# Kernel tuning notes

Measured on AMD Instinct MI355X. Metric: run time of the kernel, lower is better.

The kernel has to match this reference:

```python
import jax, jax.numpy as jnp
import numpy as np

WS = 8          # window size (== stride, non-overlapping)
C_IN = 256
RED = 8
C_QK = C_IN // RED  # 32


def setup_inputs() -> dict:
    key = jax.random.key(0)
    ks = jax.random.split(key, 8)
    B, C, H, W = 4, C_IN, 256, 256
    x = jax.random.normal(ks[0], (B, C, H, W), dtype=jnp.float32)
    # 1x1 conv weights stored as [out_ch, in_ch] (kaiming-ish scale)
    wq = jax.random.normal(ks[1], (C_QK, C), dtype=jnp.float32) * np.sqrt(2.0 / C)
    wk = jax.random.normal(ks[2], (C_QK, C), dtype=jnp.float32) * np.sqrt(2.0 / C)
    wv = jax.random.normal(ks[3], (C, C), dtype=jnp.float32) * np.sqrt(2.0 / C)
    bq = jnp.zeros((C_QK,), dtype=jnp.float32)
    bk = jnp.zeros((C_QK,), dtype=jnp.float32)
    bv = jnp.zeros((C,), dtype=jnp.float32)
    gamma = jax.random.normal(ks[4], (1,), dtype=jnp.float32) * 0.5
    return {"x": x, "wq": wq, "bq": bq, "wk": wk, "bk": bk,
            "wv": wv, "bv": bv, "gamma": gamma}


def reference(x, wq, bq, wk, bk, wv, bv, gamma):
    B, C, H, W = x.shape
    Hw, Ww = H // WS, W // WS
    P = WS * WS  # 64 pixels per window
    # extract non-overlapping windows: [B,C,H,W] -> [N, C, P]
    xw = x.reshape(B, C, Hw, WS, Ww, WS)
    xw = xw.transpose(0, 2, 4, 1, 3, 5).reshape(B * Hw * Ww, C, P)
    # 1x1 conv projections (per-pixel channel GEMM)
    q = jnp.einsum('ncp,oc->nop', xw, wq) + bq[None, :, None]   # [N, Cqk, P]
    k = jnp.einsum('ncp,oc->nop', xw, wk) + bk[None, :, None]   # [N, Cqk, P]
    v = jnp.einsum('ncp,oc->nop', xw, wv) + bv[None, :, None]   # [N, C,   P]
    # attn[p, q_] = <Q[:,p], K[:,q_]> / sqrt(P), softmax over q_
    scale = 1.0 / np.sqrt(float(P))
    attn = jax.nn.softmax(jnp.einsum('ncp,ncq->npq', q, k) * scale, axis=-1)
    # out = V @ attn^T : out[c,p] = sum_q V[c,q] * attn[p,q]
    out = jnp.einsum('ncq,npq->ncp', v, attn)  # [N, C, P]
    # merge windows back: [N, C, P] -> [B, C, H, W]
    out = out.reshape(B, Hw, Ww, C, WS, WS)
    out = out.transpose(0, 3, 1, 4, 2, 5).reshape(B, C, H, W)
    return gamma * out + x
```

## Files before the change

### kernel.cpp

```cpp
#include <hip/hip_runtime.h>
#include <hip/hip_bf16.h>
#include <stdint.h>


#define CIN    256
#define WIMG   256
#define CH_STRIDE 65536

typedef __bf16 bf16x8 __attribute__((ext_vector_type(8)));
typedef float  f32x4  __attribute__((ext_vector_type(4)));

#define XT_OFF 0
#define QT_OFF 16384
#define KT_OFF 20480
#define PT_OFF 16384
#define HALF_LDS 24576

__device__ __forceinline__ int swz8(int p) { return (p ^ (p >> 3)) & 7; }

__device__ __forceinline__ uint32_t pack2(float lo, float hi) {
  union { __bf16 h[2]; uint32_t u; } un;
  un.h[0] = (__bf16)lo; un.h[1] = (__bf16)hi;
  return un.u;
}

union fragu { uint32_t u[4]; bf16x8 v; };

__global__ __launch_bounds__(256) void wprep_kernel(
    const float* __restrict__ wq, const float* __restrict__ wk,
    const float* __restrict__ wv, __bf16* __restrict__ out)
{
  int i = blockIdx.x * 256 + threadIdx.x;
  int off = i * 4;
  const float* src;
  if (off < 8192)       src = wq + off;
  else if (off < 16384) src = wk + (off - 8192);
  else                  src = wv + (off - 16384);
  float4 v = *(const float4*)src;
  __bf16 h[4] = {(__bf16)v.x, (__bf16)v.y, (__bf16)v.z, (__bf16)v.w};
  *(uint2*)(out + off) = *(const uint2*)h;
}

__global__ __launch_bounds__(512) void win_attn_kernel(
    const float* __restrict__ x,  const __bf16* __restrict__ wsb,
    const float* __restrict__ bq, const float* __restrict__ bk,
    const float* __restrict__ bv, const float* __restrict__ gamma,
    float* __restrict__ out, int nblk)
{
  __shared__ __attribute__((aligned(16))) unsigned char lds_raw[2 * HALF_LDS];

  int t = threadIdx.x;
  int half = t >> 8;
  int tt = t & 255;
  unsigned char* ldsb = lds_raw + half * HALF_LDS;

  int bid   = blockIdx.x;
  int chunkb = nblk >> 3;
  int swz   = (bid & 7) * chunkb + (bid >> 3);
  int b   = swz >> 9;
  int hw  = (swz >> 4) & 31;
  int wwp = swz & 15;
  int ww  = wwp * 2 + half;
  size_t win_off = (size_t)b * (CIN * CH_STRIDE) + (size_t)hw * 8 * WIMG + (size_t)ww * 8;
  const float* xw = x + win_off;
  float* ow = out + win_off;

  int w = tt >> 6, l = tt & 63, l16 = l & 15, lq = l >> 4;
  float g = gamma[0];

  int qkrow = (w & 1) * 16;
  f32x4 qacc[4]    = {};
  f32x4 vacc[4][4] = {};
  const __bf16* wqkrow = wsb + ((w < 2) ? 0 : 8192) + (qkrow + l16) * 256 + lq * 8;
  const __bf16* vrow   = wsb + 16384 + (w * 64 + l16) * 256 + lq * 8;

  #pragma unroll
  for (int it = 0; it < 4; ++it) {
    int id   = it * 256 + tt;
    int hf   = id & 1;
    int i    = (id >> 1) & 7;
    int c2   = id >> 4;
    const float* r0 = xw + (size_t)(2 * c2) * CH_STRIDE + i * WIMG + hf * 4;
    float4 va = *(const float4*)r0;
    float4 vb = *(const float4*)(r0 + CH_STRIDE);
    float ax[4] = {va.x, va.y, va.z, va.w};
    float bx[4] = {vb.x, vb.y, vb.z, vb.w};
    int blk = c2 >> 2;
    int sub = (c2 & 3) * 4;
    #pragma unroll
    for (int jj = 0; jj < 4; ++jj) {
      int p = i * 8 + hf * 4 + jj;
      *(uint32_t*)(ldsb + XT_OFF + p * 256 + ((blk ^ swz8(p)) << 4) + sub) =
          pack2(ax[jj], bx[jj]);
    }
  }
  __syncthreads();

  float4 pfa[4], pfb[4];
  #pragma unroll
  for (int it = 0; it < 4; ++it) {
    int id   = it * 256 + tt;
    int hf   = id & 1;
    int i    = (id >> 1) & 7;
    int c2   = id >> 4;
    const float* r0 = xw + (size_t)(128 + 2 * c2) * CH_STRIDE + i * WIMG + hf * 4;
    pfa[it] = *(const float4*)r0;
    pfb[it] = *(const float4*)(r0 + CH_STRIDE);
  }

  #pragma unroll
  for (int ks = 0; ks < 4; ++ks) {
    bf16x8 wvf[4];
    #pragma unroll
    for (int ci = 0; ci < 4; ++ci)
      wvf[ci] = *(const bf16x8*)(vrow + ci * 16 * 256 + ks * 32);
    bf16x8 wqkf = *(const bf16x8*)(wqkrow + ks * 32);
    bf16x8 xb[4];
    #pragma unroll
    for (int qi = 0; qi < 4; ++qi) {
      int p = qi * 16 + l16;
      xb[qi] = *(const bf16x8*)(ldsb + XT_OFF + p * 256 +
                                (((ks * 4 + lq) ^ swz8(p)) << 4));
    }
    #pragma unroll
    for (int qi = 0; qi < 4; ++qi)
      qacc[qi] = __builtin_amdgcn_mfma_f32_16x16x32_bf16(wqkf, xb[qi], qacc[qi], 0, 0, 0);
    #pragma unroll
    for (int ci = 0; ci < 4; ++ci) {
      #pragma unroll
      for (int pi = 0; pi < 4; ++pi)
        vacc[pi][ci] = __builtin_amdgcn_mfma_f32_16x16x32_bf16(xb[pi], wvf[ci], vacc[pi][ci], 0, 0, 0);
    }
  }
  __syncthreads();

  #pragma unroll
  for (int it = 0; it < 4; ++it) {
    int id   = it * 256 + tt;
    int hf   = id & 1;
    int i    = (id >> 1) & 7;
    int c2   = id >> 4;
    float ax[4] = {pfa[it].x, pfa[it].y, pfa[it].z, pfa[it].w};
    float bx[4] = {pfb[it].x, pfb[it].y, pfb[it].z, pfb[it].w};
    int blk = c2 >> 2;
    int sub = (c2 & 3) * 4;
    #pragma unroll
    for (int jj = 0; jj < 4; ++jj) {
      int p = i * 8 + hf * 4 + jj;
      *(uint32_t*)(ldsb + XT_OFF + p * 256 + ((blk ^ swz8(p)) << 4) + sub) =
          pack2(ax[jj], bx[jj]);
    }
  }
  __syncthreads();

  #pragma unroll
  for (int ks = 0; ks < 4; ++ks) {
    bf16x8 wvf[4];
    #pragma unroll
    for (int ci = 0; ci < 4; ++ci)
      wvf[ci] = *(const bf16x8*)(vrow + ci * 16 * 256 + 128 + ks * 32);
    bf16x8 wqkf = *(const bf16x8*)(wqkrow + 128 + ks * 32);
    bf16x8 xb[4];
    #pragma unroll
    for (int qi = 0; qi < 4; ++qi) {
      int p = qi * 16 + l16;
      xb[qi] = *(const bf16x8*)(ldsb + XT_OFF + p * 256 +
                                (((ks * 4 + lq) ^ swz8(p)) << 4));
    }
    #pragma unroll
    for (int qi = 0; qi < 4; ++qi)
      qacc[qi] = __builtin_amdgcn_mfma_f32_16x16x32_bf16(wqkf, xb[qi], qacc[qi], 0, 0, 0);
    #pragma unroll
    for (int ci = 0; ci < 4; ++ci) {
      #pragma unroll
      for (int pi = 0; pi < 4; ++pi)
        vacc[pi][ci] = __builtin_amdgcn_mfma_f32_16x16x32_bf16(xb[pi], wvf[ci], vacc[pi][ci], 0, 0, 0);
    }
  }

  {
    const float* bias = (w < 2) ? bq : bk;
    int lbase = (w < 2) ? QT_OFF : KT_OFF;
    #pragma unroll
    for (int r = 0; r < 4; ++r) {
      int c = qkrow + lq * 4 + r;
      float bb = bias[c];
      #pragma unroll
      for (int qi = 0; qi < 4; ++qi) {
        int p = qi * 16 + l16;
        *(__bf16*)(ldsb + lbase + p * 64 + (((c >> 3) ^ (p & 3)) << 4) + (c & 7) * 2) =
            (__bf16)(qacc[qi][r] + bb);
      }
    }
  }
  __syncthreads();

  uint32_t dP[4][2];
  {
    int pq = w * 16 + l16;
    bf16x8 qa = *(const bf16x8*)(ldsb + QT_OFF + pq * 64 + ((lq ^ (pq & 3)) << 4));
    f32x4 sacc[4];
    #pragma unroll
    for (int qi = 0; qi < 4; ++qi) {
      int pk = qi * 16 + l16;
      bf16x8 kb = *(const bf16x8*)(ldsb + KT_OFF + pk * 64 + ((lq ^ (pk & 3)) << 4));
      f32x4 z = {0.f, 0.f, 0.f, 0.f};
      sacc[qi] = __builtin_amdgcn_mfma_f32_16x16x32_bf16(kb, qa, z, 0, 0, 0);
    }
    float e[4][4];
    float mx = -1e30f;
    #pragma unroll
    for (int qi = 0; qi < 4; ++qi)
      #pragma unroll
      for (int r = 0; r < 4; ++r) {
        float v = sacc[qi][r] * 0.125f;
        e[qi][r] = v;
        mx = fmaxf(mx, v);
      }
    mx = fmaxf(mx, __shfl_xor(mx, 16));
    mx = fmaxf(mx, __shfl_xor(mx, 32));
    float s = 0.f;
    #pragma unroll
    for (int qi = 0; qi < 4; ++qi)
      #pragma unroll
      for (int r = 0; r < 4; ++r) {
        e[qi][r] = __expf(e[qi][r] - mx);
        s += e[qi][r];
      }
    s += __shfl_xor(s, 16);
    s += __shfl_xor(s, 32);
    float inv = 1.0f / s;
    #pragma unroll
    for (int qi = 0; qi < 4; ++qi) {
      dP[qi][0] = pack2(e[qi][0] * inv, e[qi][1] * inv);
      dP[qi][1] = pack2(e[qi][2] * inv, e[qi][3] * inv);
    }
  }

  uint32_t dV[4][4][2];
  #pragma unroll
  for (int pi = 0; pi < 4; ++pi)
    #pragma unroll
    for (int ci = 0; ci < 4; ++ci) {
      dV[pi][ci][0] = pack2(vacc[pi][ci][0], vacc[pi][ci][1]);
      dV[pi][ci][1] = pack2(vacc[pi][ci][2], vacc[pi][ci][3]);
    }
  __syncthreads();

  {
    int q = w * 16 + l16;
    int qm = q & 7;
    #pragma unroll
    for (int qi = 0; qi < 4; ++qi) {
      int blk = (((qi >> 1) * 4) + lq) ^ qm;
      uint2 val; val.x = dP[qi][0]; val.y = dP[qi][1];
      *(uint2*)(ldsb + PT_OFF + q * 128 + blk * 16 + (qi & 1) * 8) = val;
    }
  }
  __syncthreads();

  f32x4 oacc[4][4] = {};
  #pragma unroll
  for (int ks = 0; ks < 2; ++ks) {
    bf16x8 Pf[4];
    #pragma unroll
    for (int bj = 0; bj < 4; ++bj) {
      int q = bj * 16 + l16;
      int blk = (ks * 4 + lq) ^ (q & 7);
      Pf[bj] = *(const bf16x8*)(ldsb + PT_OFF + q * 128 + blk * 16);
    }
    #pragma unroll
    for (int ci = 0; ci < 4; ++ci) {
      fragu Vf;
      Vf.u[0] = dV[2 * ks][ci][0];
      Vf.u[1] = dV[2 * ks][ci][1];
      Vf.u[2] = dV[2 * ks + 1][ci][0];
      Vf.u[3] = dV[2 * ks + 1][ci][1];
      #pragma unroll
      for (int bj = 0; bj < 4; ++bj)
        oacc[ci][bj] = __builtin_amdgcn_mfma_f32_16x16x32_bf16(Pf[bj], Vf.v, oacc[ci][bj], 0, 0, 0);
    }
  }

  #pragma unroll
  for (int ci = 0; ci < 4; ++ci) {
    int c = w * 64 + ci * 16 + l16;
    size_t cbase = (size_t)c * CH_STRIDE;
    float bvc = bv[c];
    #pragma unroll
    for (int bj = 0; bj < 4; ++bj) {
      int p0 = bj * 16 + lq * 4;
      size_t off = cbase + (size_t)(p0 >> 3) * WIMG + (p0 & 7);
      float xr[4];
      if (w >= 2) {
        int cc = c - 128;
        int blk = cc >> 3;
        int sub = ((cc >> 1) & 3) * 4 + (cc & 1) * 2;
        #pragma unroll
        for (int r = 0; r < 4; ++r) {
          int p = p0 + r;
          xr[r] = (float)(*(const __bf16*)(ldsb + XT_OFF + p * 256 +
                                           ((blk ^ swz8(p)) << 4) + sub));
        }
      } else {
        float4 xv = *(const float4*)(xw + off);
        xr[0] = xv.x; xr[1] = xv.y; xr[2] = xv.z; xr[3] = xv.w;
      }
      float4 o;
      o.x = g * (oacc[ci][bj][0] + bvc) + xr[0];
      o.y = g * (oacc[ci][bj][1] + bvc) + xr[1];
      o.z = g * (oacc[ci][bj][2] + bvc) + xr[2];
      o.w = g * (oacc[ci][bj][3] + bvc) + xr[3];
      *(float4*)(ow + off) = o;
    }
  }
}

extern "C" void kernel_launch(void* const* d_in, const int* in_sizes, int n_in,
                              void* d_out, int out_size, void* d_ws, size_t ws_size,
                              hipStream_t stream) {
  const float* x     = (const float*)d_in[0];
  const float* wq    = (const float*)d_in[1];
  const float* bq    = (const float*)d_in[2];
  const float* wk    = (const float*)d_in[3];
  const float* bk    = (const float*)d_in[4];
  const float* wv    = (const float*)d_in[5];
  const float* bv    = (const float*)d_in[6];
  const float* gamma = (const float*)d_in[7];
  float* out = (float*)d_out;
  __bf16* wsb = (__bf16*)d_ws;

  wprep_kernel<<<dim3(80), dim3(256), 0, stream>>>(wq, wk, wv, wsb);

  int B = in_sizes[0] / (CIN * CH_STRIDE);
  int nblk = B * 512;
  win_attn_kernel<<<dim3(nblk), dim3(512), 0, stream>>>(
      x, wsb, bq, bk, bv, gamma, out, nblk);
}
```

Measured before the change: 247.7 us.

## Process two window pairs per block with cross-window prefetch of next input

Each block now handles two consecutive window pairs in a loop instead of one, halving the grid. While the second channel half of the current window is being computed, the first channel half of the next window is prefetched into registers, hiding global load latency across windows. This adds register pressure and an extra barrier per iteration, and halves the number of blocks available to fill the GPU.

```diff
diff --git a/kernel.cpp b/kernel.cpp
--- a/kernel.cpp
+++ b/kernel.cpp
@@ -57,261 +57,292 @@
   int bid   = blockIdx.x;
   int chunkb = nblk >> 3;
   int swz   = (bid & 7) * chunkb + (bid >> 3);
-  int b   = swz >> 9;
-  int hw  = (swz >> 4) & 31;
-  int wwp = swz & 15;
-  int ww  = wwp * 2 + half;
-  size_t win_off = (size_t)b * (CIN * CH_STRIDE) + (size_t)hw * 8 * WIMG + (size_t)ww * 8;
-  const float* xw = x + win_off;
-  float* ow = out + win_off;
+  int b   = swz >> 8;
+  int hw  = (swz >> 3) & 31;
+  int w4  = swz & 7;
 
   int w = tt >> 6, l = tt & 63, l16 = l & 15, lq = l >> 4;
   float g = gamma[0];
 
   int qkrow = (w & 1) * 16;
-  f32x4 qacc[4]    = {};
-  f32x4 vacc[4][4] = {};
   const __bf16* wqkrow = wsb + ((w < 2) ? 0 : 8192) + (qkrow + l16) * 256 + lq * 8;
   const __bf16* vrow   = wsb + 16384 + (w * 64 + l16) * 256 + lq * 8;
 
+  int id0  = tt, id1 = 256 + tt, id2 = 512 + tt, id3 = 768 + tt;
+  float4 pfa[4], pfb[4];
+
+  size_t base_off = (size_t)b * (CIN * CH_STRIDE) + (size_t)hw * 8 * WIMG;
+
   #pragma unroll
-  for (int it = 0; it < 4; ++it) {
-    int id   = it * 256 + tt;
-    int hf   = id & 1;
-    int i    = (id >> 1) & 7;
-    int c2   = id >> 4;
-    const float* r0 = xw + (size_t)(2 * c2) * CH_STRIDE + i * WIMG + hf * 4;
-    float4 va = *(const float4*)r0;
-    float4 vb = *(const float4*)(r0 + CH_STRIDE);
-    float ax[4] = {va.x, va.y, va.z, va.w};
-    float bx[4] = {vb.x, vb.y, vb.z, vb.w};
-    int blk = c2 >> 2;
-    int sub = (c2 & 3) * 4;
-    #pragma unroll
-    for (int jj = 0; jj < 4; ++jj) {
-      int p = i * 8 + hf * 4 + jj;
-      *(uint32_t*)(ldsb + XT_OFF + p * 256 + ((blk ^ swz8(p)) << 4) + sub) =
-          pack2(ax[jj], bx[jj]);
-    }
-  }
-  __syncthreads();
-
-  float4 pfa[4], pfb[4];
-  #pragma unroll
-  for (int it = 0; it < 4; ++it) {
-    int id   = it * 256 + tt;
-    int hf   = id & 1;
-    int i    = (id >> 1) & 7;
-    int c2   = id >> 4;
-    const float* r0 = xw + (size_t)(128 + 2 * c2) * CH_STRIDE + i * WIMG + hf * 4;
-    pfa[it] = *(const float4*)r0;
-    pfb[it] = *(const float4*)(r0 + CH_STRIDE);
-  }
-
-  #pragma unroll
-  for (int ks = 0; ks < 4; ++ks) {
-    bf16x8 wvf[4];
-    #pragma unroll
-    for (int ci = 0; ci < 4; ++ci)
-      wvf[ci] = *(const bf16x8*)(vrow + ci * 16 * 256 + ks * 32);
-    bf16x8 wqkf = *(const bf16x8*)(wqkrow + ks * 32);
-    bf16x8 xb[4];
-    #pragma unroll
-    for (int qi = 0; qi < 4; ++qi) {
-      int p = qi * 16 + l16;
-      xb[qi] = *(const bf16x8*)(ldsb + XT_OFF + p * 256 +
-                                (((ks * 4 + lq) ^ swz8(p)) << 4));
-    }
-    #pragma unroll
-    for (int qi = 0; qi < 4; ++qi)
-      qacc[qi] = __builtin_amdgcn_mfma_f32_16x16x32_bf16(wqkf, xb[qi], qacc[qi], 0, 0, 0);
+  for (int p = 0; p < 2; ++p) {
+    int ww = w4 * 4 + p * 2 + half;
+    const float* xw = x + base_off + (size_t)ww * 8;
+    float* ow = out + base_off + (size_t)ww * 8;
+
+    f32x4 qacc[4]    = {};
+    f32x4 vacc[4][4] = {};
+
+    if (p == 0) {
+      #pragma unroll
+      for (int it = 0; it < 4; ++it) {
+        int id = it * 256 + tt;
+        int hf = id & 1, i = (id >> 1) & 7, c2 = id >> 4;
+        const float* r0 = xw + (size_t)(2 * c2) * CH_STRIDE + i * WIMG + hf * 4;
+        float4 va = *(const float4*)r0;
+        float4 vb = *(const float4*)(r0 + CH_STRIDE);
+        float ax[4] = {va.x, va.y, va.z, va.w};
+        float bx[4] = {vb.x, vb.y, vb.z, vb.w};
+        int blk = c2 >> 2, sub = (c2 & 3) * 4;
+        #pragma unroll
+        for (int jj = 0; jj < 4; ++jj) {
+          int px = i * 8 + hf * 4 + jj;
+          *(uint32_t*)(ldsb + XT_OFF + px * 256 + ((blk ^ swz8(px)) << 4) + sub) =
+              pack2(ax[jj], bx[jj]);
+        }
+      }
+    } else {
+      __syncthreads();
+      #pragma unroll
+      for (int it = 0; it < 4; ++it) {
+        int id = it * 256 + tt;
+        int hf = id & 1, i = (id >> 1) & 7, c2 = id >> 4;
+        float ax[4] = {pfa[it].x, pfa[it].y, pfa[it].z, pfa[it].w};
+        float bx[4] = {pfb[it].x, pfb[it].y, pfb[it].z, pfb[it].w};
+        int blk = c2 >> 2, sub = (c2 & 3) * 4;
+        #pragma unroll
+        for (int jj = 0; jj < 4; ++jj) {
+          int px = i * 8 + hf * 4 + jj;
+          *(uint32_t*)(ldsb + XT_OFF + px * 256 + ((blk ^ swz8(px)) << 4) + sub) =
+              pack2(ax[jj], bx[jj]);
+        }
+      }
+    }
+    __syncthreads();
+
+    #pragma unroll
+    for (int it = 0; it < 4; ++it) {
+      int id = it * 256 + tt;
+      int hf = id & 1, i = (id >> 1) & 7, c2 = id >> 4;
+      const float* r0 = xw + (size_t)(128 + 2 * c2) * CH_STRIDE + i * WIMG + hf * 4;
+      pfa[it] = *(const float4*)r0;
+      pfb[it] = *(const float4*)(r0 + CH_STRIDE);
+    }
+
+    #pragma unroll
+    for (int ks = 0; ks < 4; ++ks) {
+      bf16x8 wvf[4];
+      #pragma unroll
+      for (int ci = 0; ci < 4; ++ci)
+        wvf[ci] = *(const bf16x8*)(vrow + ci * 16 * 256 + ks * 32);
+      bf16x8 wqkf = *(const bf16x8*)(wqkrow + ks * 32);
+      bf16x8 xb[4];
+      #pragma unroll
+      for (int qi = 0; qi < 4; ++qi) {
+        int px = qi * 16 + l16;
+        xb[qi] = *(const bf16x8*)(ldsb + XT_OFF + px * 256 +
+                                  (((ks * 4 + lq) ^ swz8(px)) << 4));
+      }
+      #pragma unroll
+      for (int qi = 0; qi < 4; ++qi)
+        qacc[qi] = __builtin_amdgcn_mfma_f32_16x16x32_bf16(wqkf, xb[qi], qacc[qi], 0, 0, 0);
+      #pragma unroll
+      for (int ci = 0; ci < 4; ++ci) {
+        #pragma unroll
+        for (int pi = 0; pi < 4; ++pi)
+          vacc[pi][ci] = __builtin_amdgcn_mfma_f32_16x16x32_bf16(xb[pi], wvf[ci], vacc[pi][ci], 0, 0, 0);
+      }
+    }
+    __syncthreads();
+
+    #pragma unroll
+    for (int it = 0; it < 4; ++it) {
+      int id = it * 256 + tt;
+      int hf = id & 1, i = (id >> 1) & 7, c2 = id >> 4;
+      float ax[4] = {pfa[it].x, pfa[it].y, pfa[it].z, pfa[it].w};
+      float bx[4] = {pfb[it].x, pfb[it].y, pfb[it].z, pfb[it].w};
+      int blk = c2 >> 2, sub = (c2 & 3) * 4;
+      #pragma unroll
+      for (int jj = 0; jj < 4; ++jj) {
+        int px = i * 8 + hf * 4 + jj;
+        *(uint32_t*)(ldsb + XT_OFF + px * 256 + ((blk ^ swz8(px)) << 4) + sub) =
+            pack2(ax[jj], bx[jj]);
+      }
+    }
+    __syncthreads();
+
+    if (p == 0) {
+      int wwn = w4 * 4 + 2 + half;
+      const float* xn = x + base_off + (size_t)wwn * 8;
+      #pragma unroll
+      for (int it = 0; it < 4; ++it) {
+        int id = it * 256 + tt;
+        int hf = id & 1, i = (id >> 1) & 7, c2 = id >> 4;
+        const float* r0 = xn + (size_t)(2 * c2) * CH_STRIDE + i * WIMG + hf * 4;
+        pfa[it] = *(const float4*)r0;
+        pfb[it] = *(const float4*)(r0 + CH_STRIDE);
+      }
+    }
+
+    #pragma unroll
+    for (int ks = 0; ks < 4; ++ks) {
+      bf16x8 wvf[4];
+      #pragma unroll
+      for (int ci = 0; ci < 4; ++ci)
+        wvf[ci] = *(const bf16x8*)(vrow + ci * 16 * 256 + 128 + ks * 32);
+      bf16x8 wqkf = *(const bf16x8*)(wqkrow + 128 + ks * 32);
+      bf16x8 xb[4];
+      #pragma unroll
+      for (int qi = 0; qi < 4; ++qi) {
+        int px = qi * 16 + l16;
+        xb[qi] = *(const bf16x8*)(ldsb + XT_OFF + px * 256 +
+                                  (((ks * 4 + lq) ^ swz8(px)) << 4));
+      }
+      #pragma unroll
+      for (int qi = 0; qi < 4; ++qi)
+        qacc[qi] = __builtin_amdgcn_mfma_f32_16x16x32_bf16(wqkf, xb[qi], qacc[qi], 0, 0, 0);
+      #pragma unroll
+      for (int ci = 0; ci < 4; ++ci) {
+        #pragma unroll
+        for (int pi = 0; pi < 4; ++pi)
+          vacc[pi][ci] = __builtin_amdgcn_mfma_f32_16x16x32_bf16(xb[pi], wvf[ci], vacc[pi][ci], 0, 0, 0);
+      }
+    }
+
+    {
+      const float* bias = (w < 2) ? bq : bk;
+      int lbase = (w < 2) ? QT_OFF : KT_OFF;
+      #pragma unroll
+      for (int r = 0; r < 4; ++r) {
+        int c = qkrow + lq * 4 + r;
+        float bb = bias[c];
+        #pragma unroll
+        for (int qi = 0; qi < 4; ++qi) {
+          int px = qi * 16 + l16;
+          *(__bf16*)(ldsb + lbase + px * 64 + (((c >> 3) ^ (px & 3)) << 4) + (c & 7) * 2) =
+              (__bf16)(qacc[qi][r] + bb);
+        }
+      }
+    }
+    __syncthreads();
+
+    uint32_t dP[4][2];
+    {
+      int pq = w * 16 + l16;
+      bf16x8 qa = *(const bf16x8*)(ldsb + QT_OFF + pq * 64 + ((lq ^ (pq & 3)) << 4));
+      f32x4 sacc[4];
+      #pragma unroll
+      for (int qi = 0; qi < 4; ++qi) {
+        int pk = qi * 16 + l16;
+        bf16x8 kb = *(const bf16x8*)(ldsb + KT_OFF + pk * 64 + ((lq ^ (pk & 3)) << 4));
+        f32x4 z = {0.f, 0.f, 0.f, 0.f};
+        sacc[qi] = __builtin_amdgcn_mfma_f32_16x16x32_bf16(kb, qa, z, 0, 0, 0);
+      }
+      float e[4][4];
+      float mx = -1e30f;
+      #pragma unroll
+      for (int qi = 0; qi < 4; ++qi)
+        #pragma unroll
+        for (int r = 0; r < 4; ++r) {
+          float v = sacc[qi][r] * 0.125f;
+          e[qi][r] = v;
+          mx = fmaxf(mx, v);
+        }
+      mx = fmaxf(mx, __shfl_xor(mx, 16));
+      mx = fmaxf(mx, __shfl_xor(mx, 32));
+      float s = 0.f;
+      #pragma unroll
+      for (int qi = 0; qi < 4; ++qi)
+        #pragma unroll
+        for (int r = 0; r < 4; ++r) {
+          e[qi][r] = __expf(e[qi][r] - mx);
+          s += e[qi][r];
+        }
+      s += __shfl_xor(s, 16);
+      s += __shfl_xor(s, 32);
+      float inv = 1.0f / s;
+      #pragma unroll
+      for (int qi = 0; qi < 4; ++qi) {
+        dP[qi][0] = pack2(e[qi][0] * inv, e[qi][1] * inv);
+        dP[qi][1] = pack2(e[qi][2] * inv, e[qi][3] * inv);
+      }
+    }
+
+    uint32_t dV[4][4][2];
+    #pragma unroll
+    for (int pi = 0; pi < 4; ++pi)
+      #pragma unroll
+      for (int ci = 0; ci < 4; ++ci) {
+        dV[pi][ci][0] = pack2(vacc[pi][ci][0], vacc[pi][ci][1]);
+        dV[pi][ci][1] = pack2(vacc[pi][ci][2], vacc[pi][ci][3]);
+      }
+    __syncthreads();
+
+    {
+      int q = w * 16 + l16;
+      int qm = q & 7;
+      #pragma unroll
+      for (int qi = 0; qi < 4; ++qi) {
+        int blk = (((qi >> 1) * 4) + lq) ^ qm;
+        uint2 val; val.x = dP[qi][0]; val.y = dP[qi][1];
+        *(uint2*)(ldsb + PT_OFF + q * 128 + blk * 16 + (qi & 1) * 8) = val;
+      }
+    }
+    __syncthreads();
+
+    f32x4 oacc[4][4] = {};
+    #pragma unroll
+    for (int ks = 0; ks < 2; ++ks) {
+      bf16x8 Pf[4];
+      #pragma unroll
+      for (int bj = 0; bj < 4; ++bj) {
+        int q = bj * 16 + l16;
+        int blk = (ks * 4 + lq) ^ (q & 7);
+        Pf[bj] = *(const bf16x8*)(ldsb + PT_OFF + q * 128 + blk * 16);
+      }
+      #pragma unroll
+      for (int ci = 0; ci < 4; ++ci) {
+        fragu Vf;
+        Vf.u[0] = dV[2 * ks][ci][0];
+        Vf.u[1] = dV[2 * ks][ci][1];
+        Vf.u[2] = dV[2 * ks + 1][ci][0];
+        Vf.u[3] = dV[2 * ks + 1][ci][1];
+        #pragma unroll
+        for (int bj = 0; bj < 4; ++bj)
+          oacc[ci][bj] = __builtin_amdgcn_mfma_f32_16x16x32_bf16(Pf[bj], Vf.v, oacc[ci][bj], 0, 0, 0);
+      }
+    }
+
     #pragma unroll
     for (int ci = 0; ci < 4; ++ci) {
-      #pragma unroll
-      for (int pi = 0; pi < 4; ++pi)
-        vacc[pi][ci] = __builtin_amdgcn_mfma_f32_16x16x32_bf16(xb[pi], wvf[ci], vacc[pi][ci], 0, 0, 0);
-    }
-  }
-  __syncthreads();
-
-  #pragma unroll
-  for (int it = 0; it < 4; ++it) {
-    int id   = it * 256 + tt;
-    int hf   = id & 1;
-    int i    = (id >> 1) & 7;
-    int c2   = id >> 4;
-    float ax[4] = {pfa[it].x, pfa[it].y, pfa[it].z, pfa[it].w};
-    float bx[4] = {pfb[it].x, pfb[it].y, pfb[it].z, pfb[it].w};
-    int blk = c2 >> 2;
-    int sub = (c2 & 3) * 4;
-    #pragma unroll
-    for (int jj = 0; jj < 4; ++jj) {
-      int p = i * 8 + hf * 4 + jj;
-      *(uint32_t*)(ldsb + XT_OFF + p * 256 + ((blk ^ swz8(p)) << 4) + sub) =
-          pack2(ax[jj], bx[jj]);
-    }
-  }
-  __syncthreads();
-
-  #pragma unroll
-  for (int ks = 0; ks < 4; ++ks) {
-    bf16x8 wvf[4];
-    #pragma unroll
-    for (int ci = 0; ci < 4; ++ci)
-      wvf[ci] = *(const bf16x8*)(vrow + ci * 16 * 256 + 128 + ks * 32);
-    bf16x8 wqkf = *(const bf16x8*)(wqkrow + 128 + ks * 32);
-    bf16x8 xb[4];
-    #pragma unroll
-    for (int qi = 0; qi < 4; ++qi) {
-      int p = qi * 16 + l16;
-      xb[qi] = *(const bf16x8*)(ldsb + XT_OFF + p * 256 +
-                                (((ks * 4 + lq) ^ swz8(p)) << 4));
-    }
-    #pragma unroll
-    for (int qi = 0; qi < 4; ++qi)
-      qacc[qi] = __builtin_amdgcn_mfma_f32_16x16x32_bf16(wqkf, xb[qi], qacc[qi], 0, 0, 0);
-    #pragma unroll
-    for (int ci = 0; ci < 4; ++ci) {
-      #pragma unroll
-      for (int pi = 0; pi < 4; ++pi)
-        vacc[pi][ci] = __builtin_amdgcn_mfma_f32_16x16x32_bf16(xb[pi], wvf[ci], vacc[pi][ci], 0, 0, 0);
-    }
-  }
-
-  {
-    const float* bias = (w < 2) ? bq : bk;
-    int lbase = (w < 2) ? QT_OFF : KT_OFF;
-    #pragma unroll
-    for (int r = 0; r < 4; ++r) {
-      int c = qkrow + lq * 4 + r;
-      float bb = bias[c];
-      #pragma unroll
-      for (int qi = 0; qi < 4; ++qi) {
-        int p = qi * 16 + l16;
-        *(__bf16*)(ldsb + lbase + p * 64 + (((c >> 3) ^ (p & 3)) << 4) + (c & 7) * 2) =
-            (__bf16)(qacc[qi][r] + bb);
-      }
-    }
-  }
-  __syncthreads();
-
-  uint32_t dP[4][2];
-  {
-    int pq = w * 16 + l16;
-    bf16x8 qa = *(const bf16x8*)(ldsb + QT_OFF + pq * 64 + ((lq ^ (pq & 3)) << 4));
-    f32x4 sacc[4];
-    #pragma unroll
-    for (int qi = 0; qi < 4; ++qi) {
-      int pk = qi * 16 + l16;
-      bf16x8 kb = *(const bf16x8*)(ldsb + KT_OFF + pk * 64 + ((lq ^ (pk & 3)) << 4));
-      f32x4 z = {0.f, 0.f, 0.f, 0.f};
-      sacc[qi] = __builtin_amdgcn_mfma_f32_16x16x32_bf16(kb, qa, z, 0, 0, 0);
-    }
-    float e[4][4];
-    float mx = -1e30f;
-    #pragma unroll
-    for (int qi = 0; qi < 4; ++qi)
-      #pragma unroll
-      for (int r = 0; r < 4; ++r) {
-        float v = sacc[qi][r] * 0.125f;
-        e[qi][r] = v;
-        mx = fmaxf(mx, v);
-      }
-    mx = fmaxf(mx, __shfl_xor(mx, 16));
-    mx = fmaxf(mx, __shfl_xor(mx, 32));
-    float s = 0.f;
-    #pragma unroll
-    for (int qi = 0; qi < 4; ++qi)
-      #pragma unroll
-      for (int r = 0; r < 4; ++r) {
-        e[qi][r] = __expf(e[qi][r] - mx);
-        s += e[qi][r];
-      }
-    s += __shfl_xor(s, 16);
-    s += __shfl_xor(s, 32);
-    float inv = 1.0f / s;
-    #pragma unroll
-    for (int qi = 0; qi < 4; ++qi) {
-      dP[qi][0] = pack2(e[qi][0] * inv, e[qi][1] * inv);
-      dP[qi][1] = pack2(e[qi][2] * inv, e[qi][3] * inv);
-    }
-  }
-
-  uint32_t dV[4][4][2];
-  #pragma unroll
-  for (int pi = 0; pi < 4; ++pi)
-    #pragma unroll
-    for (int ci = 0; ci < 4; ++ci) {
-      dV[pi][ci][0] = pack2(vacc[pi][ci][0], vacc[pi][ci][1]);
-      dV[pi][ci][1] = pack2(vacc[pi][ci][2], vacc[pi][ci][3]);
-    }
-  __syncthreads();
-
-  {
-    int q = w * 16 + l16;
-    int qm = q & 7;
-    #pragma unroll
-    for (int qi = 0; qi < 4; ++qi) {
-      int blk = (((qi >> 1) * 4) + lq) ^ qm;
-      uint2 val; val.x = dP[qi][0]; val.y = dP[qi][1];
-      *(uint2*)(ldsb + PT_OFF + q * 128 + blk * 16 + (qi & 1) * 8) = val;
-    }
-  }
-  __syncthreads();
-
-  f32x4 oacc[4][4] = {};
-  #pragma unroll
-  for (int ks = 0; ks < 2; ++ks) {
-    bf16x8 Pf[4];
-    #pragma unroll
-    for (int bj = 0; bj < 4; ++bj) {
-      int q = bj * 16 + l16;
-      int blk = (ks * 4 + lq) ^ (q & 7);
-      Pf[bj] = *(const bf16x8*)(ldsb + PT_OFF + q * 128 + blk * 16);
-    }
-    #pragma unroll
-    for (int ci = 0; ci < 4; ++ci) {
-      fragu Vf;
-      Vf.u[0] = dV[2 * ks][ci][0];
-      Vf.u[1] = dV[2 * ks][ci][1];
-      Vf.u[2] = dV[2 * ks + 1][ci][0];
-      Vf.u[3] = dV[2 * ks + 1][ci][1];
-      #pragma unroll
-      for (int bj = 0; bj < 4; ++bj)
-        oacc[ci][bj] = __builtin_amdgcn_mfma_f32_16x16x32_bf16(Pf[bj], Vf.v, oacc[ci][bj], 0, 0, 0);
-    }
-  }
-
-  #pragma unroll
-  for (int ci = 0; ci < 4; ++ci) {
-    int c = w * 64 + ci * 16 + l16;
-    size_t cbase = (size_t)c * CH_STRIDE;
-    float bvc = bv[c];
-    #pragma unroll
-    for (int bj = 0; bj < 4; ++bj) {
-      int p0 = bj * 16 + lq * 4;
-      size_t off = cbase + (size_t)(p0 >> 3) * WIMG + (p0 & 7);
-      float xr[4];
-      if (w >= 2) {
-        int cc = c - 128;
-        int blk = cc >> 3;
-        int sub = ((cc >> 1) & 3) * 4 + (cc & 1) * 2;
-        #pragma unroll
-        for (int r = 0; r < 4; ++r) {
-          int p = p0 + r;
-          xr[r] = (float)(*(const __bf16*)(ldsb + XT_OFF + p * 256 +
-                                           ((blk ^ swz8(p)) << 4) + sub));
-        }
-      } else {
-        float4 xv = *(const float4*)(xw + off);
-        xr[0] = xv.x; xr[1] = xv.y; xr[2] = xv.z; xr[3] = xv.w;
-      }
-      float4 o;
-      o.x = g * (oacc[ci][bj][0] + bvc) + xr[0];
-      o.y = g * (oacc[ci][bj][1] + bvc) + xr[1];
-      o.z = g * (oacc[ci][bj][2] + bvc) + xr[2];
-      o.w = g * (oacc[ci][bj][3] + bvc) + xr[3];
-      *(float4*)(ow + off) = o;
+      int c = w * 64 + ci * 16 + l16;
+      size_t cbase = (size_t)c * CH_STRIDE;
+      float bvc = bv[c];
+      #pragma unroll
+      for (int bj = 0; bj < 4; ++bj) {
+        int p0 = bj * 16 + lq * 4;
+        size_t off = cbase + (size_t)(p0 >> 3) * WIMG + (p0 & 7);
+        float xr[4];
+        if (w >= 2) {
+          int cc = c - 128;
+          int blk = cc >> 3;
+          int sub = ((cc >> 1) & 3) * 4 + (cc & 1) * 2;
+          #pragma unroll
+          for (int r = 0; r < 4; ++r) {
+            int px = p0 + r;
+            xr[r] = (float)(*(const __bf16*)(ldsb + XT_OFF + px * 256 +
+                                             ((blk ^ swz8(px)) << 4) + sub));
+          }
+        } else {
+          float4 xv = *(const float4*)(xw + off);
+          xr[0] = xv.x; xr[1] = xv.y; xr[2] = xv.z; xr[3] = xv.w;
+        }
+        float4 o;
+        o.x = g * (oacc[ci][bj][0] + bvc) + xr[0];
+        o.y = g * (oacc[ci][bj][1] + bvc) + xr[1];
+        o.z = g * (oacc[ci][bj][2] + bvc) + xr[2];
+        o.w = g * (oacc[ci][bj][3] + bvc) + xr[3];
+        *(float4*)(ow + off) = o;
+      }
     }
   }
 }
@@ -333,7 +364,7 @@
   wprep_kernel<<<dim3(80), dim3(256), 0, stream>>>(wq, wk, wv, wsb);
 
   int B = in_sizes[0] / (CIN * CH_STRIDE);
-  int nblk = B * 512;
+  int nblk = B * 256;
   win_attn_kernel<<<dim3(nblk), dim3(512), 0, stream>>>(
       x, wsb, bq, bk, bv, gamma, out, nblk);
 }
```

Result: slower. 362.7 us (+46.4%).
